# Performance work log

Hardware: AMD Instinct MI355X
Metric: run time of the kernel (lower is better)

Reference implementation:

```python
import jax, jax.numpy as jnp
import numpy as np

NODE_DIM = 128
EDGE_DIM = 16
HIDDEN = 128
B = 2
N = 20000
M = 320000


def setup_inputs() -> dict:
    key = jax.random.key(0)
    ks = jax.random.split(key, 20)

    def w(k, shape):
        return (jax.random.normal(k, shape, jnp.float32) / jnp.sqrt(shape[0])).astype(jnp.float32)

    X = jax.random.normal(ks[0], (B, N, NODE_DIM), jnp.float32)
    E = jax.random.normal(ks[1], (B, M, EDGE_DIM), jnp.float32)
    edges = jax.random.randint(ks[2], (B, M, 2), 0, N)
    return {
        "X": X, "E": E, "edges": edges,
        # node_mlp: Linear(node_dim,hidden) -> ReLU -> Linear(hidden,hidden)
        "nW1": w(ks[3], (NODE_DIM, HIDDEN)), "nb1": jnp.zeros((HIDDEN,), jnp.float32),
        "nW2": w(ks[4], (HIDDEN, HIDDEN)), "nb2": jnp.zeros((HIDDEN,), jnp.float32),
        # edge_mlp: Linear(2*node_dim+edge_dim,hidden) -> ReLU -> Linear(hidden,hidden)
        "eW1": w(ks[5], (2 * NODE_DIM + EDGE_DIM, HIDDEN)), "eb1": jnp.zeros((HIDDEN,), jnp.float32),
        "eW2": w(ks[6], (HIDDEN, HIDDEN)), "eb2": jnp.zeros((HIDDEN,), jnp.float32),
        # edge_proj: Linear(edge_dim, hidden)
        "pW": w(ks[7], (EDGE_DIM, HIDDEN)), "pb": jnp.zeros((HIDDEN,), jnp.float32),
        # read: Linear(2*hidden,64) -> ReLU -> Linear(64,2)
        "rW1": w(ks[8], (2 * HIDDEN, 64)), "rb1": jnp.zeros((64,), jnp.float32),
        "rW2": w(ks[9], (64, 2)), "rb2": jnp.zeros((2,), jnp.float32),
        "gate_scale": jnp.float32(2.0),
    }


def _forward_one(X, E, edges, nW1, nb1, nW2, nb2, eW1, eb1, eW2, eb2,
                 pW, pb, rW1, rb1, rW2, rb2, gate_scale):
    n_nodes = X.shape[0]
    n_edges = E.shape[0]
    # Hx = relu(node_mlp(X))  (node_mlp already ends without activation)
    Hx = jax.nn.relu(jax.nn.relu(X @ nW1 + nb1) @ nW2 + nb2)  # [N, H]
    # gate from 3rd edge-feature column (edge_dim >= 3)
    gate = jnp.clip(1.0 + gate_scale * E[:, 2:3], 0.0, 3.0)  # [M, 1]
    src = edges[:, 0]
    dst = edges[:, 1]
    # per-edge message: concat(X[i], X[j], E[k]) -> MLP -> relu -> * gate
    eij = jnp.concatenate([X[src], X[dst], E], axis=-1)  # [M, 2*node_dim+edge_dim]
    m = jax.nn.relu(jax.nn.relu(eij @ eW1 + eb1) @ eW2 + eb2) * gate  # [M, H]
    # scatter-add to both endpoints (sum order irrelevant)
    agg = (jax.ops.segment_sum(m, src, num_segments=n_nodes)
           + jax.ops.segment_sum(m, dst, num_segments=n_nodes))  # [N, H]
    # edge context: mean of gated edge projections
    edge_ctx = jnp.sum(gate * (E @ pW + pb), axis=0) / (n_edges + 1e-6)  # [H]
    H = Hx + agg
    feat = jnp.concatenate([H.mean(axis=0), edge_ctx], axis=0)  # [2H]
    return jax.nn.relu(feat @ rW1 + rb1) @ rW2 + rb2  # [2]


def reference(X, E, edges, nW1, nb1, nW2, nb2, eW1, eb1, eW2, eb2,
              pW, pb, rW1, rb1, rW2, rb2, gate_scale):
    fn = jax.vmap(_forward_one, in_axes=(0, 0, 0) + (None,) * 15)
    return fn(X, E, edges, nW1, nb1, nW2, nb2, eW1, eb1, eW2, eb2,
              pW, pb, rW1, rb1, rW2, rb2, gate_scale)  # [B, 2]
```

## Files before the change

### kernel.cpp

```cpp
#include <hip/hip_runtime.h>

typedef short bf16x8 __attribute__((ext_vector_type(8)));
typedef float f32x4 __attribute__((ext_vector_type(4)));

#define NB 2
#define NN 20000
#define ME 320000
#define STRIPES 64
#define NT 8

__device__ __forceinline__ unsigned short f2bf(float f) {
  union { float f; unsigned int u; } v; v.f = f;
  unsigned int r = (v.u + 0x7FFFu + ((v.u >> 16) & 1u)) >> 16;
  return (unsigned short)r;
}

__device__ __forceinline__ bf16x8 pack2(float4 a, float4 b) {
  bf16x8 v;
  v[0]=(short)f2bf(a.x); v[1]=(short)f2bf(a.y); v[2]=(short)f2bf(a.z); v[3]=(short)f2bf(a.w);
  v[4]=(short)f2bf(b.x); v[5]=(short)f2bf(b.y); v[6]=(short)f2bf(b.z); v[7]=(short)f2bf(b.w);
  return v;
}

__device__ __forceinline__ f32x4 mfma16(bf16x8 a, bf16x8 b, f32x4 c) {
  return __builtin_amdgcn_mfma_f32_16x16x32_bf16(a, b, c, 0, 0, 0);
}

__global__ void prep_w_kernel(const float* __restrict__ eW1, const float* __restrict__ eW2,
                              const float* __restrict__ nW1, const float* __restrict__ nW2,
                              const float* __restrict__ pW,
                              short* __restrict__ ew1T, short* __restrict__ ew2T,
                              short* __restrict__ nw1T, short* __restrict__ nw2T,
                              short* __restrict__ pwT) {
  int c = blockIdx.x;
  int t = threadIdx.x;
  for (int k = t; k < 288; k += 256)
    ew1T[c * 288 + k] = (k < 272) ? (short)f2bf(eW1[(size_t)k * 128 + c]) : (short)0;
  if (t < 128) {
    ew2T[c * 128 + t] = (short)f2bf(eW2[(size_t)t * 128 + c]);
    nw1T[c * 128 + t] = (short)f2bf(nW1[(size_t)t * 128 + c]);
    nw2T[c * 128 + t] = (short)f2bf(nW2[(size_t)t * 128 + c]);
  }
  if (t < 32) pwT[c * 32 + t] = (t < 16) ? (short)f2bf(pW[(size_t)t * 128 + c]) : (short)0;
}


template<bool WRITEBF>
__global__ __launch_bounds__(256, 2) void node_kernel(
    const float* __restrict__ X, short* __restrict__ Xbf,
    const short* __restrict__ nw1T, const short* __restrict__ nw2T,
    const float* __restrict__ nb1, const float* __restrict__ nb2,
    float* __restrict__ node_acc) {
  __shared__ __align__(16) short A_lds[64 * 136];
  __shared__ __align__(16) short h1_lds[64 * 136];
  const int tid = threadIdx.x;
  const int lane = tid & 63;
  const int w = tid >> 6;
  const int fc = lane & 15;
  const int fg = lane >> 4;
  const int ncol0 = w * 32;
  const int b = blockIdx.y;
  const float* X_b = X + (size_t)b * NN * 128;
  short* Xbf_b = Xbf + (size_t)b * NN * 128;

  bf16x8 B1[2][4], B2[2][4];
  float b1v[2], b2v[2];
#pragma unroll
  for (int nt = 0; nt < 2; ++nt) {
    int col = ncol0 + nt * 16 + fc;
#pragma unroll
    for (int kt = 0; kt < 4; ++kt) {
      B1[nt][kt] = *reinterpret_cast<const bf16x8*>(nw1T + col * 128 + kt * 32 + fg * 8);
      B2[nt][kt] = *reinterpret_cast<const bf16x8*>(nw2T + col * 128 + kt * 32 + fg * 8);
    }
    b1v[nt] = nb1[col];
    b2v[nt] = nb2[col];
  }

  const int n0 = blockIdx.x * 64;
#pragma unroll
  for (int p = 0; p < 8; ++p) {
    int slot = p * 256 + tid;
    int row = slot >> 5, chunk = slot & 31;
    int node = n0 + row;
    ushort4 v = {0, 0, 0, 0};
    if (node < NN) {
      float4 f = *reinterpret_cast<const float4*>(X_b + (size_t)node * 128 + chunk * 4);
      v.x = f2bf(f.x); v.y = f2bf(f.y); v.z = f2bf(f.z); v.w = f2bf(f.w);
      if (WRITEBF) *reinterpret_cast<ushort4*>(Xbf_b + (size_t)node * 128 + chunk * 4) = v;
    }
    *reinterpret_cast<ushort4*>(&A_lds[row * 136 + chunk * 4]) = v;
  }
  __syncthreads();

  f32x4 zf = {0.f, 0.f, 0.f, 0.f};
  float acc0 = 0.f, acc1 = 0.f;
#pragma unroll
  for (int rt = 0; rt < 4; ++rt) {
    const short* arow = &A_lds[(rt * 16 + fc) * 136 + fg * 8];
    f32x4 a0 = zf, a1 = zf;
#pragma unroll
    for (int kt = 0; kt < 4; ++kt) {
      bf16x8 av = *reinterpret_cast<const bf16x8*>(arow + kt * 32);
      a0 = mfma16(av, B1[0][kt], a0);
      a1 = mfma16(av, B1[1][kt], a1);
    }
#pragma unroll
    for (int r = 0; r < 4; ++r) {
      int row = rt * 16 + fg * 4 + r;
      h1_lds[row * 136 + ncol0 + fc] = (short)f2bf(fmaxf(a0[r] + b1v[0], 0.f));
      h1_lds[row * 136 + ncol0 + 16 + fc] = (short)f2bf(fmaxf(a1[r] + b1v[1], 0.f));
    }
  }
  __syncthreads();
#pragma unroll
  for (int rt = 0; rt < 4; ++rt) {
    const short* hrow = &h1_lds[(rt * 16 + fc) * 136 + fg * 8];
    f32x4 a0 = zf, a1 = zf;
#pragma unroll
    for (int kt = 0; kt < 4; ++kt) {
      bf16x8 hv = *reinterpret_cast<const bf16x8*>(hrow + kt * 32);
      a0 = mfma16(hv, B2[0][kt], a0);
      a1 = mfma16(hv, B2[1][kt], a1);
    }
#pragma unroll
    for (int r = 0; r < 4; ++r) {
      int row = n0 + rt * 16 + fg * 4 + r;
      if (row < NN) {
        acc0 += fmaxf(a0[r] + b2v[0], 0.f);
        acc1 += fmaxf(a1[r] + b2v[1], 0.f);
      }
    }
  }
  acc0 += __shfl_xor(acc0, 16); acc0 += __shfl_xor(acc0, 32);
  acc1 += __shfl_xor(acc1, 16); acc1 += __shfl_xor(acc1, 32);
  if (fg == 0) {
    const int stripe = blockIdx.x & (STRIPES - 1);
    float* base = node_acc + ((size_t)b * STRIPES + stripe) * 128;
    atomicAdd(base + ncol0 + fc, acc0);
    atomicAdd(base + ncol0 + 16 + fc, acc1);
  }
}


template<bool XBF>
__global__ __launch_bounds__(256, 2) void edge_kernel(
    const short* __restrict__ Xbf, const float* __restrict__ X,
    const float* __restrict__ E, const int* __restrict__ edges,
    const short* __restrict__ ew1T, const short* __restrict__ ew2T,
    const short* __restrict__ pwT, const float* __restrict__ eb1,
    const float* __restrict__ eb2, const float* __restrict__ gsp,
    float* __restrict__ edge_acc) {
  __shared__ __align__(16) short A_lds[64 * 296];
  __shared__ __align__(16) short h1_lds[64 * 136];
  __shared__ float gate_lds[2][64];
  __shared__ int idx_lds[2][128];

  const int tid = threadIdx.x;
  const int lane = tid & 63;
  const int w = tid >> 6;
  const int fc = lane & 15;
  const int fg = lane >> 4;
  const int ncol0 = w * 32;
  const int b = blockIdx.y;

  const float gs = gsp[0];
  const float* E_b = E + (size_t)b * ME * 16;
  const int* edges_b = edges + (size_t)b * ME * 2;
  const short* Xbf_b = Xbf + (size_t)b * NN * 128;
  const float* X_b = X + (size_t)b * NN * 128;
  const int tile0 = blockIdx.x * NT;

  bf16x8 B1[2][9], B2[2][4], PWf[2];
  float eb1v[2], eb2v[2];
#pragma unroll
  for (int nt = 0; nt < 2; ++nt) {
    int col = ncol0 + nt * 16 + fc;
#pragma unroll
    for (int kt = 0; kt < 9; ++kt)
      B1[nt][kt] = *reinterpret_cast<const bf16x8*>(ew1T + col * 288 + kt * 32 + fg * 8);
#pragma unroll
    for (int kt = 0; kt < 4; ++kt)
      B2[nt][kt] = *reinterpret_cast<const bf16x8*>(ew2T + col * 128 + kt * 32 + fg * 8);
    PWf[nt] = *reinterpret_cast<const bf16x8*>(pwT + col * 32 + fg * 8);
    eb1v[nt] = eb1[col];
    eb2v[nt] = eb2[col];
  }

  const int grow = tid >> 1;
  const int ge = grow & 63;
  const int gsd = grow >> 6;
  const int gpos = (ge << 1) | gsd;
  const int ghalf = tid & 1;
  const int et = tid >> 2, q = tid & 3;

#define GATHER8(node, v0, v1, v2, v3, v4, v5, v6, v7)                                   \
  if (XBF) {                                                                            \
    const bf16x8* gp = reinterpret_cast<const bf16x8*>(Xbf_b + (size_t)(node)*128 + ghalf*64); \
    v0 = gp[0]; v1 = gp[1]; v2 = gp[2]; v3 = gp[3];                                     \
    v4 = gp[4]; v5 = gp[5]; v6 = gp[6]; v7 = gp[7];                                     \
  } else {                                                                              \
    const float4* gp = reinterpret_cast<const float4*>(X_b + (size_t)(node)*128 + ghalf*64); \
    v0 = pack2(gp[0], gp[1]);  v1 = pack2(gp[2], gp[3]);                                \
    v2 = pack2(gp[4], gp[5]);  v3 = pack2(gp[6], gp[7]);                                \
    v4 = pack2(gp[8], gp[9]);  v5 = pack2(gp[10], gp[11]);                              \
    v6 = pack2(gp[12], gp[13]); v7 = pack2(gp[14], gp[15]);                             \
  }

#define STORE8(v0, v1, v2, v3, v4, v5, v6, v7)                                          \
  {                                                                                     \
    bf16x8* aw8 = reinterpret_cast<bf16x8*>(&A_lds[ge * 296 + gsd * 128 + ghalf * 64]); \
    aw8[0] = v0; aw8[1] = v1; aw8[2] = v2; aw8[3] = v3;                                 \
    aw8[4] = v4; aw8[5] = v5; aw8[6] = v6; aw8[7] = v7;                                 \
  }

  if (tid < 64) {
    bf16x8 z = {0, 0, 0, 0, 0, 0, 0, 0};
    *reinterpret_cast<bf16x8*>(&A_lds[tid * 296 + 272]) = z;
    *reinterpret_cast<bf16x8*>(&A_lds[tid * 296 + 280]) = z;
  }
  {
    const int e0 = tile0 * 64;
    int node = edges_b[(size_t)e0 * 2 + gpos];
    bf16x8 s0, s1, s2, s3, s4, s5, s6, s7;
    GATHER8(node, s0, s1, s2, s3, s4, s5, s6, s7);
    STORE8(s0, s1, s2, s3, s4, s5, s6, s7);
    float4 ev = *reinterpret_cast<const float4*>(E_b + (size_t)e0 * 16 + tid * 4);
    ushort4 evb; evb.x = f2bf(ev.x); evb.y = f2bf(ev.y); evb.z = f2bf(ev.z); evb.w = f2bf(ev.w);
    *reinterpret_cast<ushort4*>(&A_lds[et * 296 + 256 + q * 4]) = evb;
    if (q == 0) gate_lds[0][et] = fminf(fmaxf(1.f + gs * ev.z, 0.f), 3.f);
    if (tid < 128) idx_lds[1][tid] = edges_b[(size_t)(tile0 + 1) * 64 * 2 + tid];
  }
  __syncthreads();

  float accm0 = 0.f, accm1 = 0.f, accp0 = 0.f, accp1 = 0.f, accg = 0.f;
  const f32x4 zf = {0.f, 0.f, 0.f, 0.f};

  for (int it = 0; it < NT; ++it) {
    const int cur = it & 1, nxt = (it + 1) & 1;
    const bool hasn1 = (it + 1 < NT);
    const bool hasn2 = (it + 2 < NT);
    const int e0n = (hasn1 ? (tile0 + it + 1) : tile0) * 64;
    const int e0n2 = (hasn2 ? (tile0 + it + 2) : tile0) * 64;

    float4 epre = *reinterpret_cast<const float4*>(E_b + (size_t)e0n * 16 + tid * 4);
    int idxpre = 0;
    if (tid < 128) idxpre = edges_b[(size_t)e0n2 * 2 + tid];
    const int node = idx_lds[nxt][gpos];
    bf16x8 p0v, p1v, p2v, p3v, p4v, p5v, p6v, p7v;
    GATHER8(node, p0v, p1v, p2v, p3v, p4v, p5v, p6v, p7v);

#pragma unroll
    for (int rt = 0; rt < 4; ++rt) {
      const short* arow = &A_lds[(rt * 16 + fc) * 296 + fg * 8];
      f32x4 a0 = zf, a1 = zf;
#pragma unroll
      for (int kt = 0; kt < 9; ++kt) {
        bf16x8 av = *reinterpret_cast<const bf16x8*>(arow + kt * 32);
        a0 = mfma16(av, B1[0][kt], a0);
        a1 = mfma16(av, B1[1][kt], a1);
      }
      bf16x8 av8 = *reinterpret_cast<const bf16x8*>(arow + 256);
      f32x4 q0 = mfma16(av8, PWf[0], zf);
      f32x4 q1 = mfma16(av8, PWf[1], zf);
#pragma unroll
      for (int r = 0; r < 4; ++r) {
        int row = rt * 16 + fg * 4 + r;
        float g = gate_lds[cur][row];
        accp0 += q0[r] * g;
        accp1 += q1[r] * g;
        h1_lds[row * 136 + ncol0 + fc] = (short)f2bf(fmaxf(a0[r] + eb1v[0], 0.f));
        h1_lds[row * 136 + ncol0 + 16 + fc] = (short)f2bf(fmaxf(a1[r] + eb1v[1], 0.f));
      }
    }
    __syncthreads();

    if (hasn1) {
      STORE8(p0v, p1v, p2v, p3v, p4v, p5v, p6v, p7v);
      ushort4 evb; evb.x = f2bf(epre.x); evb.y = f2bf(epre.y); evb.z = f2bf(epre.z); evb.w = f2bf(epre.w);
      *reinterpret_cast<ushort4*>(&A_lds[et * 296 + 256 + q * 4]) = evb;
      if (q == 0) gate_lds[nxt][et] = fminf(fmaxf(1.f + gs * epre.z, 0.f), 3.f);
      if (tid < 128) idx_lds[cur][tid] = idxpre;
    }

    if (w == 0) accg += gate_lds[cur][lane];
#pragma unroll
    for (int rt = 0; rt < 4; ++rt) {
      const short* hrow = &h1_lds[(rt * 16 + fc) * 136 + fg * 8];
      f32x4 a0 = zf, a1 = zf;
#pragma unroll
      for (int kt = 0; kt < 4; ++kt) {
        bf16x8 hv = *reinterpret_cast<const bf16x8*>(hrow + kt * 32);
        a0 = mfma16(hv, B2[0][kt], a0);
        a1 = mfma16(hv, B2[1][kt], a1);
      }
#pragma unroll
      for (int r = 0; r < 4; ++r) {
        int row = rt * 16 + fg * 4 + r;
        float g = gate_lds[cur][row];
        accm0 += fmaxf(a0[r] + eb2v[0], 0.f) * g;
        accm1 += fmaxf(a1[r] + eb2v[1], 0.f) * g;
      }
    }
    __syncthreads();
  }

  accm0 += __shfl_xor(accm0, 16); accm0 += __shfl_xor(accm0, 32);
  accm1 += __shfl_xor(accm1, 16); accm1 += __shfl_xor(accm1, 32);
  accp0 += __shfl_xor(accp0, 16); accp0 += __shfl_xor(accp0, 32);
  accp1 += __shfl_xor(accp1, 16); accp1 += __shfl_xor(accp1, 32);
  const int stripe = blockIdx.x & (STRIPES - 1);
  float* base = edge_acc + ((size_t)b * STRIPES + stripe) * 264;
  if (fg == 0) {
    atomicAdd(base + ncol0 + fc, accm0);
    atomicAdd(base + ncol0 + 16 + fc, accm1);
    atomicAdd(base + 128 + ncol0 + fc, accp0);
    atomicAdd(base + 128 + ncol0 + 16 + fc, accp1);
  }
  if (w == 0) {
#pragma unroll
    for (int off = 1; off < 64; off <<= 1) accg += __shfl_xor(accg, off);
    if (lane == 0) atomicAdd(base + 256, accg);
  }
#undef GATHER8
#undef STORE8
}


__global__ void final_kernel(const float* __restrict__ edge_acc, const float* __restrict__ node_acc,
                             const float* __restrict__ pb, const float* __restrict__ rW1,
                             const float* __restrict__ rb1, const float* __restrict__ rW2,
                             const float* __restrict__ rb2, float* __restrict__ out) {
  int b = blockIdx.x;
  int j = threadIdx.x;
  __shared__ float feat[256];
  __shared__ float h[64];
  const float* ea = edge_acc + (size_t)b * STRIPES * 264;
  const float* na = node_acc + (size_t)b * STRIPES * 128;
  float ms = 0.f, ps = 0.f, hs = 0.f, gsum = 0.f;
  for (int s = 0; s < STRIPES; ++s) {
    ms += ea[s * 264 + j];
    ps += ea[s * 264 + 128 + j];
    hs += na[s * 128 + j];
    gsum += ea[s * 264 + 256];
  }
  feat[j] = (hs + 2.f * ms) * (1.f / (float)NN);
  feat[128 + j] = (ps + gsum * pb[j]) / ((float)ME + 1e-6f);
  __syncthreads();
  if (j < 64) {
    float a = rb1[j];
    for (int i = 0; i < 256; ++i) a += feat[i] * rW1[i * 64 + j];
    h[j] = fmaxf(a, 0.f);
  }
  __syncthreads();
  if (j < 2) {
    float a = rb2[j];
    for (int i = 0; i < 64; ++i) a += h[i] * rW2[i * 2 + j];
    out[b * 2 + j] = a;
  }
}


extern "C" void kernel_launch(void* const* d_in, const int* in_sizes, int n_in,
                              void* d_out, int out_size, void* d_ws, size_t ws_size,
                              hipStream_t stream) {
  const float* X = (const float*)d_in[0];
  const float* E = (const float*)d_in[1];
  const int* edges = (const int*)d_in[2];
  const float* nW1 = (const float*)d_in[3];
  const float* nb1 = (const float*)d_in[4];
  const float* nW2 = (const float*)d_in[5];
  const float* nb2 = (const float*)d_in[6];
  const float* eW1 = (const float*)d_in[7];
  const float* eb1 = (const float*)d_in[8];
  const float* eW2 = (const float*)d_in[9];
  const float* eb2 = (const float*)d_in[10];
  const float* pW = (const float*)d_in[11];
  const float* pb = (const float*)d_in[12];
  const float* rW1 = (const float*)d_in[13];
  const float* rb1 = (const float*)d_in[14];
  const float* rW2 = (const float*)d_in[15];
  const float* rb2 = (const float*)d_in[16];
  const float* gscale = (const float*)d_in[17];
  float* out = (float*)d_out;

  char* ws = (char*)d_ws;
  size_t off = 0;
  auto alloc = [&](size_t sz) -> void* {
    void* p = ws + off;
    off = (off + sz + 255) & ~(size_t)255;
    return p;
  };
  short* ew1T = (short*)alloc(288 * 128 * 2);
  short* ew2T = (short*)alloc(128 * 128 * 2);
  short* nw1T = (short*)alloc(128 * 128 * 2);
  short* nw2T = (short*)alloc(128 * 128 * 2);
  short* pwT  = (short*)alloc(32 * 128 * 2);
  size_t acc_floats = (size_t)NB * STRIPES * 264 + (size_t)NB * STRIPES * 128;
  float* acc = (float*)alloc(acc_floats * 4);
  float* edge_acc = acc;
  float* node_acc = acc + (size_t)NB * STRIPES * 264;
  size_t xbf_bytes = (size_t)NB * NN * 128 * 2;
  size_t off_before_xbf = off;
  short* Xbf = (short*)alloc(xbf_bytes);
  bool use_xbf = (off_before_xbf + xbf_bytes) <= ws_size;

  hipMemsetAsync(acc, 0, acc_floats * 4, stream);
  prep_w_kernel<<<dim3(128), dim3(256), 0, stream>>>(eW1, eW2, nW1, nW2, pW,
                                                     ew1T, ew2T, nw1T, nw2T, pwT);
  if (use_xbf) {
    node_kernel<true><<<dim3(313, 2), dim3(256), 0, stream>>>(X, Xbf, nw1T, nw2T, nb1, nb2, node_acc);
    edge_kernel<true><<<dim3(625, 2), dim3(256), 0, stream>>>(
        Xbf, X, E, edges, ew1T, ew2T, pwT, eb1, eb2, gscale, edge_acc);
  } else {
    node_kernel<false><<<dim3(313, 2), dim3(256), 0, stream>>>(X, Xbf, nw1T, nw2T, nb1, nb2, node_acc);
    edge_kernel<false><<<dim3(625, 2), dim3(256), 0, stream>>>(
        Xbf, X, E, edges, ew1T, ew2T, pwT, eb1, eb2, gscale, edge_acc);
  }
  final_kernel<<<dim3(NB), dim3(128), 0, stream>>>(edge_acc, node_acc, pb, rW1, rb1, rW2, rb2, out);
}
```

Measured before the change: 235.4 us.

## Precompute per-node first-layer projections so edges gather projected rows

The first edge-MLP layer is split algebraically. X@W_src and X@W_dst are computed once per node in the node kernel and stored as fp32 Xs/Xd. The edge kernel then gathers these projected rows and adds them to a small E@W_e MFMA, removing the 256-wide K from the per-edge GEMM. The cost is larger fp32 intermediate buffers (two extra N×128 arrays) and fp32 gathers in place of bf16 ones. Hidden columns are permuted so each lane can fetch float2 pairs, and h1 goes through a swizzled LDS layout. The old path is kept as a fallback for when the workspace is too small.

Result: slower. 395.1 us (+67.8%).

```diff
diff --git a/kernel.cpp b/kernel.cpp
--- a/kernel.cpp
+++ b/kernel.cpp
@@ -7,7 +7,8 @@
 #define NN 20000
 #define ME 320000
 #define STRIPES 64
-#define NT 8
+#define NT_FB 8
+#define NT2 5
 
 __device__ __forceinline__ unsigned short f2bf(float f) {
   union { float f; unsigned int u; } v; v.f = f;
@@ -26,12 +27,339 @@
   return __builtin_amdgcn_mfma_f32_16x16x32_bf16(a, b, c, 0, 0, 0);
 }
 
-__global__ void prep_w_kernel(const float* __restrict__ eW1, const float* __restrict__ eW2,
-                              const float* __restrict__ nW1, const float* __restrict__ nW2,
-                              const float* __restrict__ pW,
-                              short* __restrict__ ew1T, short* __restrict__ ew2T,
-                              short* __restrict__ nw1T, short* __restrict__ nw2T,
-                              short* __restrict__ pwT) {
+__device__ __forceinline__ int hidcol(int c) {
+  return (c & ~31) + 2 * (c & 15) + ((c >> 4) & 1);
+}
+
+
+__global__ void prep_w2(const float* __restrict__ eW1, const float* __restrict__ eW2,
+                        const float* __restrict__ nW1, const float* __restrict__ nW2,
+                        const float* __restrict__ pW,
+                        short* __restrict__ es1T, short* __restrict__ ed1T,
+                        short* __restrict__ w1eT, short* __restrict__ ew2T,
+                        short* __restrict__ nw1T, short* __restrict__ nw2T,
+                        short* __restrict__ pwT) {
+  int c = blockIdx.x;
+  int t = threadIdx.x;
+  int hc = hidcol(c);
+  if (t < 128) {
+    es1T[c * 128 + t] = (short)f2bf(eW1[(size_t)t * 128 + hc]);
+    ed1T[c * 128 + t] = (short)f2bf(eW1[(size_t)(128 + t) * 128 + hc]);
+    ew2T[c * 128 + t] = (short)f2bf(eW2[(size_t)t * 128 + c]);
+    nw1T[c * 128 + t] = (short)f2bf(nW1[(size_t)t * 128 + c]);
+    nw2T[c * 128 + t] = (short)f2bf(nW2[(size_t)t * 128 + c]);
+  }
+  if (t < 32) {
+    w1eT[c * 32 + t] = (t < 16) ? (short)f2bf(eW1[(size_t)(256 + t) * 128 + hc]) : (short)0;
+    pwT[c * 32 + t]  = (t < 16) ? (short)f2bf(pW[(size_t)t * 128 + c]) : (short)0;
+  }
+}
+
+__global__ __launch_bounds__(256, 4) void node_prep(
+    const float* __restrict__ X,
+    const short* __restrict__ nw1T, const short* __restrict__ nw2T,
+    const short* __restrict__ es1T, const short* __restrict__ ed1T,
+    const float* __restrict__ nb1, const float* __restrict__ nb2,
+    float* __restrict__ Xs, float* __restrict__ Xd,
+    float* __restrict__ node_acc) {
+  __shared__ __align__(16) short A_lds[64 * 136];
+  __shared__ __align__(16) short B_lds[64 * 136];
+  const int tid = threadIdx.x;
+  const int lane = tid & 63;
+  const int w = tid >> 6;
+  const int fc = lane & 15;
+  const int fg = lane >> 4;
+  const int ncol0 = w * 32;
+  const int b = blockIdx.y;
+  const int n0 = blockIdx.x * 64;
+  const float* X_b = X + (size_t)b * NN * 128;
+  float* Xs_b = Xs + (size_t)b * NN * 128;
+  float* Xd_b = Xd + (size_t)b * NN * 128;
+  const f32x4 zf = {0.f, 0.f, 0.f, 0.f};
+
+#pragma unroll
+  for (int p = 0; p < 8; ++p) {
+    int slot = p * 256 + tid;
+    int row = slot >> 5, chunk = slot & 31;
+    int node = n0 + row;
+    uint2 v = {0, 0};
+    if (node < NN) {
+      float4 f = *(const float4*)(X_b + (size_t)node * 128 + chunk * 4);
+      v.x = (unsigned)f2bf(f.x) | ((unsigned)f2bf(f.y) << 16);
+      v.y = (unsigned)f2bf(f.z) | ((unsigned)f2bf(f.w) << 16);
+    }
+    *(uint2*)(&A_lds[row * 136 + chunk * 4]) = v;
+  }
+  __syncthreads();
+
+  {
+    bf16x8 BS[2][4];
+#pragma unroll
+    for (int nt = 0; nt < 2; ++nt)
+#pragma unroll
+      for (int kt = 0; kt < 4; ++kt)
+        BS[nt][kt] = *(const bf16x8*)(es1T + (ncol0 + nt * 16 + fc) * 128 + kt * 32 + fg * 8);
+#pragma unroll
+    for (int rt = 0; rt < 4; ++rt) {
+      f32x4 a0 = zf, a1 = zf;
+#pragma unroll
+      for (int kt = 0; kt < 4; ++kt) {
+        bf16x8 av = *(const bf16x8*)(&A_lds[(rt * 16 + fc) * 136 + kt * 32 + fg * 8]);
+        a0 = mfma16(av, BS[0][kt], a0);
+        a1 = mfma16(av, BS[1][kt], a1);
+      }
+#pragma unroll
+      for (int r = 0; r < 4; ++r) {
+        int node = n0 + rt * 16 + fg * 4 + r;
+        if (node < NN) {
+          float2 o; o.x = a0[r]; o.y = a1[r];
+          *(float2*)(Xs_b + (size_t)node * 128 + ncol0 + 2 * fc) = o;
+        }
+      }
+    }
+  }
+  {
+    bf16x8 BD[2][4];
+#pragma unroll
+    for (int nt = 0; nt < 2; ++nt)
+#pragma unroll
+      for (int kt = 0; kt < 4; ++kt)
+        BD[nt][kt] = *(const bf16x8*)(ed1T + (ncol0 + nt * 16 + fc) * 128 + kt * 32 + fg * 8);
+#pragma unroll
+    for (int rt = 0; rt < 4; ++rt) {
+      f32x4 a0 = zf, a1 = zf;
+#pragma unroll
+      for (int kt = 0; kt < 4; ++kt) {
+        bf16x8 av = *(const bf16x8*)(&A_lds[(rt * 16 + fc) * 136 + kt * 32 + fg * 8]);
+        a0 = mfma16(av, BD[0][kt], a0);
+        a1 = mfma16(av, BD[1][kt], a1);
+      }
+#pragma unroll
+      for (int r = 0; r < 4; ++r) {
+        int node = n0 + rt * 16 + fg * 4 + r;
+        if (node < NN) {
+          float2 o; o.x = a0[r]; o.y = a1[r];
+          *(float2*)(Xd_b + (size_t)node * 128 + ncol0 + 2 * fc) = o;
+        }
+      }
+    }
+  }
+  {
+    float b1v0 = nb1[ncol0 + fc], b1v1 = nb1[ncol0 + 16 + fc];
+    bf16x8 BN[2][4];
+#pragma unroll
+    for (int nt = 0; nt < 2; ++nt)
+#pragma unroll
+      for (int kt = 0; kt < 4; ++kt)
+        BN[nt][kt] = *(const bf16x8*)(nw1T + (ncol0 + nt * 16 + fc) * 128 + kt * 32 + fg * 8);
+#pragma unroll
+    for (int rt = 0; rt < 4; ++rt) {
+      f32x4 a0 = {b1v0, b1v0, b1v0, b1v0};
+      f32x4 a1 = {b1v1, b1v1, b1v1, b1v1};
+#pragma unroll
+      for (int kt = 0; kt < 4; ++kt) {
+        bf16x8 av = *(const bf16x8*)(&A_lds[(rt * 16 + fc) * 136 + kt * 32 + fg * 8]);
+        a0 = mfma16(av, BN[0][kt], a0);
+        a1 = mfma16(av, BN[1][kt], a1);
+      }
+#pragma unroll
+      for (int r = 0; r < 4; ++r) {
+        int row = rt * 16 + fg * 4 + r;
+        B_lds[row * 136 + ncol0 + fc] = (short)f2bf(fmaxf(a0[r], 0.f));
+        B_lds[row * 136 + ncol0 + 16 + fc] = (short)f2bf(fmaxf(a1[r], 0.f));
+      }
+    }
+  }
+  __syncthreads();
+
+  float acc0 = 0.f, acc1 = 0.f;
+  {
+    float b2v0 = nb2[ncol0 + fc], b2v1 = nb2[ncol0 + 16 + fc];
+    bf16x8 BN2[2][4];
+#pragma unroll
+    for (int nt = 0; nt < 2; ++nt)
+#pragma unroll
+      for (int kt = 0; kt < 4; ++kt)
+        BN2[nt][kt] = *(const bf16x8*)(nw2T + (ncol0 + nt * 16 + fc) * 128 + kt * 32 + fg * 8);
+#pragma unroll
+    for (int rt = 0; rt < 4; ++rt) {
+      f32x4 a0 = {b2v0, b2v0, b2v0, b2v0};
+      f32x4 a1 = {b2v1, b2v1, b2v1, b2v1};
+#pragma unroll
+      for (int kt = 0; kt < 4; ++kt) {
+        bf16x8 hv = *(const bf16x8*)(&B_lds[(rt * 16 + fc) * 136 + kt * 32 + fg * 8]);
+        a0 = mfma16(hv, BN2[0][kt], a0);
+        a1 = mfma16(hv, BN2[1][kt], a1);
+      }
+#pragma unroll
+      for (int r = 0; r < 4; ++r) {
+        int node = n0 + rt * 16 + fg * 4 + r;
+        if (node < NN) {
+          acc0 += fmaxf(a0[r], 0.f);
+          acc1 += fmaxf(a1[r], 0.f);
+        }
+      }
+    }
+  }
+  acc0 += __shfl_xor(acc0, 16); acc0 += __shfl_xor(acc0, 32);
+  acc1 += __shfl_xor(acc1, 16); acc1 += __shfl_xor(acc1, 32);
+  if (fg == 0) {
+    const int stripe = blockIdx.x & (STRIPES - 1);
+    float* base = node_acc + ((size_t)b * STRIPES + stripe) * 128;
+    atomicAdd(base + ncol0 + fc, acc0);
+    atomicAdd(base + ncol0 + 16 + fc, acc1);
+  }
+}
+
+__global__ __launch_bounds__(256, 4) void edge_kernel3(
+    const float* __restrict__ Xs, const float* __restrict__ Xd,
+    const float* __restrict__ E, const int* __restrict__ edges,
+    const short* __restrict__ w1eT, const short* __restrict__ pwT,
+    const short* __restrict__ ew2T, const float* __restrict__ eb1,
+    const float* __restrict__ eb2, const float* __restrict__ gsp,
+    float* __restrict__ edge_acc) {
+  __shared__ __align__(16) short h1s[64 * 128];
+  __shared__ __align__(16) short E_lds[64 * 40];
+  __shared__ float gate_lds[64];
+  __shared__ __align__(8) int idx_lds[128];
+
+  const int tid = threadIdx.x;
+  const int lane = tid & 63;
+  const int w = tid >> 6;
+  const int fc = lane & 15;
+  const int fg = lane >> 4;
+  const int ncol0 = w * 32;
+  const int b = blockIdx.y;
+  const float gs = gsp[0];
+  const float* E_b = E + (size_t)b * ME * 16;
+  const int* edges_b = edges + (size_t)b * ME * 2;
+  const float* Xs_b = Xs + (size_t)b * NN * 128;
+  const float* Xd_b = Xd + (size_t)b * NN * 128;
+  const f32x4 zf = {0.f, 0.f, 0.f, 0.f};
+
+  bf16x8 W1E[2], PW[2], B2f[2][4];
+  float eb1v[2], eb2v[2];
+#pragma unroll
+  for (int nt = 0; nt < 2; ++nt) {
+    int col = ncol0 + nt * 16 + fc;
+    W1E[nt] = *(const bf16x8*)(w1eT + col * 32 + fg * 8);
+    PW[nt] = *(const bf16x8*)(pwT + col * 32 + fg * 8);
+#pragma unroll
+    for (int kt = 0; kt < 4; ++kt)
+      B2f[nt][kt] = *(const bf16x8*)(ew2T + col * 128 + kt * 32 + fg * 8);
+    eb1v[nt] = eb1[ncol0 + 2 * fc + nt];
+    eb2v[nt] = eb2[col];
+  }
+
+  if (tid < 64) {
+    uint4 z = {0, 0, 0, 0};
+    *(uint4*)(&E_lds[tid * 40 + 16]) = z;
+    *(uint4*)(&E_lds[tid * 40 + 24]) = z;
+  }
+
+  const int et = tid >> 2, eq = tid & 3;
+  const int cb = ncol0 + 2 * fc;
+  float accm0 = 0.f, accm1 = 0.f, accp0 = 0.f, accp1 = 0.f, accg = 0.f;
+
+  for (int it = 0; it < NT2; ++it) {
+    const int e0 = (blockIdx.x * NT2 + it) * 64;
+    if (tid < 128) idx_lds[tid] = edges_b[(size_t)e0 * 2 + tid];
+    {
+      float4 fe = ((const float4*)E_b)[(size_t)(e0 + et) * 4 + eq];
+      uint2 ue;
+      ue.x = (unsigned)f2bf(fe.x) | ((unsigned)f2bf(fe.y) << 16);
+      ue.y = (unsigned)f2bf(fe.z) | ((unsigned)f2bf(fe.w) << 16);
+      *(uint2*)(&E_lds[et * 40 + eq * 4]) = ue;
+      if (eq == 0) gate_lds[et] = fminf(fmaxf(1.f + gs * fe.z, 0.f), 3.f);
+    }
+    __syncthreads();
+
+    float2 gsv[2][4], gdv[2][4];
+#define LOAD_RT(P, RT)                                                        \
+    {                                                                         \
+      _Pragma("unroll")                                                       \
+      for (int r = 0; r < 4; ++r) {                                           \
+        int row = (RT) * 16 + fg * 4 + r;                                     \
+        int2 sd = *(const int2*)(&idx_lds[2 * row]);                          \
+        gsv[P][r] = *(const float2*)(Xs_b + (size_t)sd.x * 128 + cb);         \
+        gdv[P][r] = *(const float2*)(Xd_b + (size_t)sd.y * 128 + cb);         \
+      }                                                                       \
+    }
+    LOAD_RT(0, 0)
+#pragma unroll
+    for (int rt = 0; rt < 4; ++rt) {
+      if (rt < 3) LOAD_RT((rt + 1) & 1, rt + 1)
+      bf16x8 Ef = *(const bf16x8*)(&E_lds[(rt * 16 + fc) * 40 + fg * 8]);
+      f32x4 a0 = {eb1v[0], eb1v[0], eb1v[0], eb1v[0]};
+      f32x4 a1 = {eb1v[1], eb1v[1], eb1v[1], eb1v[1]};
+      a0 = mfma16(Ef, W1E[0], a0);
+      a1 = mfma16(Ef, W1E[1], a1);
+      f32x4 q0 = mfma16(Ef, PW[0], zf);
+      f32x4 q1 = mfma16(Ef, PW[1], zf);
+#pragma unroll
+      for (int r = 0; r < 4; ++r) {
+        int row = rt * 16 + fg * 4 + r;
+        float g = gate_lds[row];
+        accp0 += q0[r] * g;
+        accp1 += q1[r] * g;
+        float v0 = fmaxf(a0[r] + gsv[rt & 1][r].x + gdv[rt & 1][r].x, 0.f);
+        float v1 = fmaxf(a1[r] + gsv[rt & 1][r].y + gdv[rt & 1][r].y, 0.f);
+        int di = row * 64 + ((w * 16 + fc) ^ ((row & 7) << 2));
+        ((unsigned*)h1s)[di] = (unsigned)f2bf(v0) | ((unsigned)f2bf(v1) << 16);
+      }
+    }
+#undef LOAD_RT
+    __syncthreads();
+
+    if (w == 0) accg += gate_lds[lane];
+#pragma unroll
+    for (int rt = 0; rt < 4; ++rt) {
+      const int arow = rt * 16 + fc;
+      f32x4 a0 = {eb2v[0], eb2v[0], eb2v[0], eb2v[0]};
+      f32x4 a1 = {eb2v[1], eb2v[1], eb2v[1], eb2v[1]};
+#pragma unroll
+      for (int kt = 0; kt < 4; ++kt) {
+        bf16x8 hv = *(const bf16x8*)(&h1s[arow * 128 + ((kt * 32 + fg * 8) ^ ((arow & 7) << 3))]);
+        a0 = mfma16(hv, B2f[0][kt], a0);
+        a1 = mfma16(hv, B2f[1][kt], a1);
+      }
+#pragma unroll
+      for (int r = 0; r < 4; ++r) {
+        int row = rt * 16 + fg * 4 + r;
+        float g = gate_lds[row];
+        accm0 += fmaxf(a0[r], 0.f) * g;
+        accm1 += fmaxf(a1[r], 0.f) * g;
+      }
+    }
+    __syncthreads();
+  }
+
+  accm0 += __shfl_xor(accm0, 16); accm0 += __shfl_xor(accm0, 32);
+  accm1 += __shfl_xor(accm1, 16); accm1 += __shfl_xor(accm1, 32);
+  accp0 += __shfl_xor(accp0, 16); accp0 += __shfl_xor(accp0, 32);
+  accp1 += __shfl_xor(accp1, 16); accp1 += __shfl_xor(accp1, 32);
+  const int stripe = blockIdx.x & (STRIPES - 1);
+  float* base = edge_acc + ((size_t)b * STRIPES + stripe) * 264;
+  if (fg == 0) {
+    atomicAdd(base + ncol0 + fc, accm0);
+    atomicAdd(base + ncol0 + 16 + fc, accm1);
+    atomicAdd(base + 128 + ncol0 + fc, accp0);
+    atomicAdd(base + 128 + ncol0 + 16 + fc, accp1);
+  }
+  if (w == 0) {
+#pragma unroll
+    for (int off = 1; off < 64; off <<= 1) accg += __shfl_xor(accg, off);
+    if (lane == 0) atomicAdd(base + 256, accg);
+  }
+}
+
+
+__global__ void prep_w_fb(const float* __restrict__ eW1, const float* __restrict__ eW2,
+                          const float* __restrict__ nW1, const float* __restrict__ nW2,
+                          const float* __restrict__ pW,
+                          short* __restrict__ ew1T, short* __restrict__ ew2T,
+                          short* __restrict__ nw1T, short* __restrict__ nw2T,
+                          short* __restrict__ pwT) {
   int c = blockIdx.x;
   int t = threadIdx.x;
   for (int k = t; k < 288; k += 256)
@@ -44,9 +372,8 @@
   if (t < 32) pwT[c * 32 + t] = (t < 16) ? (short)f2bf(pW[(size_t)t * 128 + c]) : (short)0;
 }
 
-
 template<bool WRITEBF>
-__global__ __launch_bounds__(256, 2) void node_kernel(
+__global__ __launch_bounds__(256, 2) void node_kernel_fb(
     const float* __restrict__ X, short* __restrict__ Xbf,
     const short* __restrict__ nw1T, const short* __restrict__ nw2T,
     const float* __restrict__ nb1, const float* __restrict__ nb2,
@@ -142,9 +469,8 @@
   }
 }
 
-
 template<bool XBF>
-__global__ __launch_bounds__(256, 2) void edge_kernel(
+__global__ __launch_bounds__(256, 2) void edge_kernel_fb(
     const short* __restrict__ Xbf, const float* __restrict__ X,
     const float* __restrict__ E, const int* __restrict__ edges,
     const short* __restrict__ ew1T, const short* __restrict__ ew2T,
@@ -169,7 +495,7 @@
   const int* edges_b = edges + (size_t)b * ME * 2;
   const short* Xbf_b = Xbf + (size_t)b * NN * 128;
   const float* X_b = X + (size_t)b * NN * 128;
-  const int tile0 = blockIdx.x * NT;
+  const int tile0 = blockIdx.x * NT_FB;
 
   bf16x8 B1[2][9], B2[2][4], PWf[2];
   float eb1v[2], eb2v[2];
@@ -236,10 +562,10 @@
   float accm0 = 0.f, accm1 = 0.f, accp0 = 0.f, accp1 = 0.f, accg = 0.f;
   const f32x4 zf = {0.f, 0.f, 0.f, 0.f};
 
-  for (int it = 0; it < NT; ++it) {
+  for (int it = 0; it < NT_FB; ++it) {
     const int cur = it & 1, nxt = (it + 1) & 1;
-    const bool hasn1 = (it + 1 < NT);
-    const bool hasn2 = (it + 2 < NT);
+    const bool hasn1 = (it + 1 < NT_FB);
+    const bool hasn2 = (it + 2 < NT_FB);
     const int e0n = (hasn1 ? (tile0 + it + 1) : tile0) * 64;
     const int e0n2 = (hasn2 ? (tile0 + it + 2) : tile0) * 64;
 
@@ -391,31 +717,59 @@
     off = (off + sz + 255) & ~(size_t)255;
     return p;
   };
-  short* ew1T = (short*)alloc(288 * 128 * 2);
+  size_t acc_floats = (size_t)NB * STRIPES * 264 + (size_t)NB * STRIPES * 128;
+
+  short* es1T = (short*)alloc(128 * 128 * 2);
+  short* ed1T = (short*)alloc(128 * 128 * 2);
+  short* w1eT = (short*)alloc(128 * 32 * 2);
   short* ew2T = (short*)alloc(128 * 128 * 2);
   short* nw1T = (short*)alloc(128 * 128 * 2);
   short* nw2T = (short*)alloc(128 * 128 * 2);
-  short* pwT  = (short*)alloc(32 * 128 * 2);
-  size_t acc_floats = (size_t)NB * STRIPES * 264 + (size_t)NB * STRIPES * 128;
-  float* acc = (float*)alloc(acc_floats * 4);
-  float* edge_acc = acc;
-  float* node_acc = acc + (size_t)NB * STRIPES * 264;
+  short* pwT  = (short*)alloc(128 * 32 * 2);
+  float* acc  = (float*)alloc(acc_floats * 4);
+  float* Xs   = (float*)alloc((size_t)NB * NN * 128 * 4);
+  float* Xd   = (float*)alloc((size_t)NB * NN * 128 * 4);
+  bool fit = off <= ws_size;
+
+  if (fit) {
+    float* edge_acc = acc;
+    float* node_acc = acc + (size_t)NB * STRIPES * 264;
+    hipMemsetAsync(acc, 0, acc_floats * 4, stream);
+    prep_w2<<<dim3(128), dim3(256), 0, stream>>>(eW1, eW2, nW1, nW2, pW,
+                                                 es1T, ed1T, w1eT, ew2T, nw1T, nw2T, pwT);
+    node_prep<<<dim3(313, 2), dim3(256), 0, stream>>>(X, nw1T, nw2T, es1T, ed1T,
+                                                      nb1, nb2, Xs, Xd, node_acc);
+    edge_kernel3<<<dim3(1000, 2), dim3(256), 0, stream>>>(Xs, Xd, E, edges, w1eT, pwT,
+                                                          ew2T, eb1, eb2, gscale, edge_acc);
+    final_kernel<<<dim3(NB), dim3(128), 0, stream>>>(edge_acc, node_acc, pb, rW1, rb1, rW2, rb2, out);
+    return;
+  }
+
+  off = 0;
+  short* ew1T_f = (short*)alloc(288 * 128 * 2);
+  short* ew2T_f = (short*)alloc(128 * 128 * 2);
+  short* nw1T_f = (short*)alloc(128 * 128 * 2);
+  short* nw2T_f = (short*)alloc(128 * 128 * 2);
+  short* pwT_f  = (short*)alloc(32 * 128 * 2);
+  float* acc_f  = (float*)alloc(acc_floats * 4);
+  float* edge_acc = acc_f;
+  float* node_acc = acc_f + (size_t)NB * STRIPES * 264;
   size_t xbf_bytes = (size_t)NB * NN * 128 * 2;
   size_t off_before_xbf = off;
   short* Xbf = (short*)alloc(xbf_bytes);
   bool use_xbf = (off_before_xbf + xbf_bytes) <= ws_size;
 
-  hipMemsetAsync(acc, 0, acc_floats * 4, stream);
-  prep_w_kernel<<<dim3(128), dim3(256), 0, stream>>>(eW1, eW2, nW1, nW2, pW,
-                                                     ew1T, ew2T, nw1T, nw2T, pwT);
+  hipMemsetAsync(acc_f, 0, acc_floats * 4, stream);
+  prep_w_fb<<<dim3(128), dim3(256), 0, stream>>>(eW1, eW2, nW1, nW2, pW,
+                                                 ew1T_f, ew2T_f, nw1T_f, nw2T_f, pwT_f);
   if (use_xbf) {
-    node_kernel<true><<<dim3(313, 2), dim3(256), 0, stream>>>(X, Xbf, nw1T, nw2T, nb1, nb2, node_acc);
-    edge_kernel<true><<<dim3(625, 2), dim3(256), 0, stream>>>(
-        Xbf, X, E, edges, ew1T, ew2T, pwT, eb1, eb2, gscale, edge_acc);
+    node_kernel_fb<true><<<dim3(313, 2), dim3(256), 0, stream>>>(X, Xbf, nw1T_f, nw2T_f, nb1, nb2, node_acc);
+    edge_kernel_fb<true><<<dim3(625, 2), dim3(256), 0, stream>>>(
+        Xbf, X, E, edges, ew1T_f, ew2T_f, pwT_f, eb1, eb2, gscale, edge_acc);
   } else {
-    node_kernel<false><<<dim3(313, 2), dim3(256), 0, stream>>>(X, Xbf, nw1T, nw2T, nb1, nb2, node_acc);
-    edge_kernel<false><<<dim3(625, 2), dim3(256), 0, stream>>>(
-        Xbf, X, E, edges, ew1T, ew2T, pwT, eb1, eb2, gscale, edge_acc);
+    node_kernel_fb<false><<<dim3(313, 2), dim3(256), 0, stream>>>(X, Xbf, nw1T_f, nw2T_f, nb1, nb2, node_acc);
+    edge_kernel_fb<false><<<dim3(625, 2), dim3(256), 0, stream>>>(
+        Xbf, X, E, edges, ew1T_f, ew2T_f, pwT_f, eb1, eb2, gscale, edge_acc);
   }
   final_kernel<<<dim3(NB), dim3(128), 0, stream>>>(edge_acc, node_acc, pb, rW1, rb1, rW2, rb2, out);
 }
```
